# Optimization experiments

Measured on AMD Instinct MI355X. Metric: run time of the kernel, lower is better.

## Reference

```python
import jax, jax.numpy as jnp
import numpy as np
import itertools, math

M_MODES = 10
N_PHOT = 5
IN_MODES = np.array([0, 2, 4, 6, 8])  # input_state = [1,0,1,0,...], 5 photons
INV_SQRT2 = 0.7071067811865476

# Fock output bases (lexicographic ordering)
ROWS_NB = np.array(list(itertools.combinations(range(M_MODES), N_PHOT)), np.int32)          # [252,5] no-bunching
ROWS_B = np.array(list(itertools.combinations_with_replacement(range(M_MODES), N_PHOT)), np.int32)  # [2002,5] bunched

def _norms(rows):
    out = []
    for r in rows:
        c = np.bincount(r, minlength=M_MODES)
        out.append(float(np.prod([math.factorial(int(v)) for v in c])))
    return np.array(out, np.float32)

NORM_NB = _norms(ROWS_NB)  # all ones
NORM_B = _norms(ROWS_B)

# Glynn sign vectors for n=5 permanents (delta_0 fixed to +1): [16,5]
_D = np.array(list(itertools.product([1.0, -1.0], repeat=N_PHOT - 1)), np.float32)
DELTAS = np.concatenate([np.ones((_D.shape[0], 1), np.float32), _D], axis=1)
DSIGNS = np.prod(DELTAS, axis=1)


def _mzi(t1, t2):
    # BS // PS(t1) // BS // PS(t2); BS = (1/sqrt2)[[1,i],[i,1]], PS on first mode of pair
    B = jnp.array([[1.0, 1.0j], [1.0j, 1.0]], dtype=jnp.complex64) * INV_SQRT2
    e1 = jnp.exp(1j * t1)
    e2 = jnp.exp(1j * t2)
    M1 = B * jnp.stack([e1, jnp.ones_like(e1)])[:, None]   # PS(t1) @ BS
    M2 = B @ M1                                            # BS @ ...
    return M2 * jnp.stack([e2, jnp.ones_like(e2)])[:, None]  # PS(t2) @ ...


def interferometer(phases):
    """Rectangular (Clements) mesh on 10 modes with 45 MZIs; phases [45,2] -> U [10,10] complex."""
    Ts = jax.vmap(lambda p: _mzi(p[0], p[1]))(phases)  # [45,2,2]
    U = jnp.eye(M_MODES, dtype=jnp.complex64)
    k = 0
    for layer in range(M_MODES):
        for p in range(layer % 2, M_MODES - 1, 2):
            U = U.at[p:p + 2, :].set(Ts[k] @ U[p:p + 2, :])
            k += 1
    return U


def batched_permanent(Ms):
    """Glynn formula for [...,5,5] complex matrices."""
    D = jnp.asarray(DELTAS, dtype=Ms.dtype)       # [16,5]
    s = jnp.asarray(DSIGNS, dtype=Ms.dtype)       # [16]
    rowsum = jnp.einsum('di,...ij->...dj', D, Ms)  # [...,16,5]
    return jnp.einsum('d,...d->...', s, jnp.prod(rowsum, axis=-1)) / (2 ** (N_PHOT - 1))


def fock_probs(U, rows, norm):
    """U [B,10,10]; rows [K,5] output-mode indices (with repetition for bunching); norm [K]."""
    M = U[:, rows][..., IN_MODES]        # [B,K,5,5]
    perm = batched_permanent(M)          # [B,K]
    return (jnp.abs(perm) ** 2) / jnp.asarray(norm)


def _forward(x, W_down, b_down, phases_l1, phases_r1, phases_lf, phases_rf, W_out, b_out):
    h = (x @ W_down + b_down) / jnp.pi                 # downscale + DivideByPi -> [B,10]
    WL1 = interferometer(phases_l1)
    WR1 = interferometer(phases_r1)
    U1 = jnp.einsum('mk,bk,kn->bmn', WR1, jnp.exp(1j * h), WL1)  # WR @ diag(e^{i phi}) @ WL
    e1 = fock_probs(U1, ROWS_NB, NORM_NB)              # [B,252], no_bunching=True
    # final circuit: 252 px phase shifters round-robin over 10 modes -> phases add per mode
    Bsz = e1.shape[0]
    pad = jnp.pad(e1, ((0, 0), (0, 260 - 252)))
    phi2 = pad.reshape(Bsz, 26, M_MODES).sum(axis=1)   # [B,10]
    WLF = interferometer(phases_lf)
    WRF = interferometer(phases_rf)
    UF = jnp.einsum('mk,bk,kn->bmn', WRF, jnp.exp(1j * phi2), WLF)
    probs = fock_probs(UF, ROWS_B, NORM_B)             # [B,2002], bunched Fock states
    return probs @ W_out + b_out                       # [B,num_classes]


def setup_inputs() -> dict:
    key = jax.random.key(0)
    ks = jax.random.split(key, 9)
    two_pi = 2.0 * np.pi
    return {
        'x': jax.random.normal(ks[0], (128, 784), dtype=jnp.float32),
        'W_down': jax.random.normal(ks[1], (784, 10), dtype=jnp.float32) * 0.05,
        'b_down': jax.random.normal(ks[2], (10,), dtype=jnp.float32) * 0.05,
        'phases_l1': jax.random.uniform(ks[3], (45, 2), dtype=jnp.float32) * two_pi,
        'phases_r1': jax.random.uniform(ks[4], (45, 2), dtype=jnp.float32) * two_pi,
        'phases_lf': jax.random.uniform(ks[5], (45, 2), dtype=jnp.float32) * two_pi,
        'phases_rf': jax.random.uniform(ks[6], (45, 2), dtype=jnp.float32) * two_pi,
        'W_out': jax.random.normal(ks[7], (2002, 10), dtype=jnp.float32) * 0.02,
        'b_out': jax.random.normal(ks[8], (10,), dtype=jnp.float32) * 0.02,
    }


def reference(x, W_down, b_down, phases_l1, phases_r1, phases_lf, phases_rf, W_out, b_out):
    return _forward(x, W_down, b_down, phases_l1, phases_r1, phases_lf, phases_rf, W_out, b_out)
```

## Files before the change

### kernel.cpp

```cpp
#include <hip/hip_runtime.h>
#include <math.h>


#define PI_F 3.14159265358979323846f

__constant__ int BINOM[14][5] = {
  {1, 0, 0, 0, 0},  {1, 1, 0, 0, 0},  {1, 2, 1, 0, 0},   {1, 3, 3, 1, 0},
  {1, 4, 6, 4, 1},  {1, 5,10,10, 5},  {1, 6,15,20,15},   {1, 7,21,35,35},
  {1, 8,28,56,70},  {1, 9,36,84,126}, {1,10,45,120,210}, {1,11,55,165,330},
  {1,12,66,220,495},{1,13,78,286,715}
};
__constant__ float FACTF[6] = {1.f, 1.f, 2.f, 6.f, 24.f, 120.f};

__device__ __forceinline__ float2 cmul(float2 a, float2 b) {
  return make_float2(fmaf(a.x, b.x, -a.y * b.y), fmaf(a.x, b.y, a.y * b.x));
}
__device__ __forceinline__ float2 cadd(float2 a, float2 b) {
  return make_float2(a.x + b.x, a.y + b.y);
}
__device__ __forceinline__ float2 cscale(float2 a, float s) {
  return make_float2(a.x * s, a.y * s);
}
__device__ __forceinline__ float2 imul(float2 a) {
  return make_float2(-a.y, a.x);
}

template <int N>
__device__ __forceinline__ void unrank5(int r, int c[5]) {
  int x = 0;
#pragma unroll
  for (int i = 0; i < 5; i++) {
    for (;;) {
      int cnt = BINOM[N - 1 - x][4 - i];
      if (r < cnt) { c[i] = x; x++; break; }
      r -= cnt; x++;
    }
  }
}

__device__ __forceinline__ float2 perm5(const float2 M[5][5]) {
  float2 rs[5];
#pragma unroll
  for (int j = 0; j < 5; j++) {
    rs[j] = M[0][j];
#pragma unroll
    for (int i = 1; i < 5; i++) rs[j] = cadd(rs[j], M[i][j]);
  }
  float2 acc = cmul(cmul(cmul(cmul(rs[0], rs[1]), rs[2]), rs[3]), rs[4]);
#pragma unroll
  for (int t = 1; t < 16; t++) {
    const int g = t ^ (t >> 1);
    const int bit = (t & 1) ? 0 : ((t & 2) ? 1 : ((t & 4) ? 2 : 3));
    const int i = bit + 1;
    const float step = ((g >> bit) & 1) ? -2.0f : 2.0f;
#pragma unroll
    for (int j = 0; j < 5; j++) {
      rs[j].x = fmaf(step, M[i][j].x, rs[j].x);
      rs[j].y = fmaf(step, M[i][j].y, rs[j].y);
    }
    float2 p = cmul(cmul(cmul(cmul(rs[0], rs[1]), rs[2]), rs[3]), rs[4]);
    const float s = (__popc(g) & 1) ? -1.0f : 1.0f;
    acc.x = fmaf(s, p.x, acc.x);
    acc.y = fmaf(s, p.y, acc.y);
  }
  return make_float2(acc.x * (1.0f / 16.0f), acc.y * (1.0f / 16.0f));
}

__global__ __launch_bounds__(256) void k_head(
    const float* __restrict__ x, const float* __restrict__ Wd,
    const float* __restrict__ bd, const float* __restrict__ ph_l1,
    const float* __restrict__ ph_r1, const float* __restrict__ ph_lf,
    const float* __restrict__ ph_rf, float* __restrict__ h,
    float2* __restrict__ Umats) {
  const int tid = threadIdx.x;
  __shared__ float red[4][10];
  __shared__ float2 T[45][4];
  __shared__ float2 U[100];

  if (blockIdx.x < 128) {
    const int b = blockIdx.x;
    float acc[10];
#pragma unroll
    for (int c = 0; c < 10; c++) acc[c] = 0.f;
    for (int i = tid; i < 784; i += 256) {
      float xv = x[b * 784 + i];
      const float* w = Wd + i * 10;
#pragma unroll
      for (int c = 0; c < 10; c++) acc[c] = fmaf(xv, w[c], acc[c]);
    }
    const int lane = tid & 63, wave = tid >> 6;
#pragma unroll
    for (int c = 0; c < 10; c++) {
      float r = acc[c];
#pragma unroll
      for (int d = 32; d > 0; d >>= 1) r += __shfl_down(r, d);
      if (lane == 0) red[wave][c] = r;
    }
    __syncthreads();
    if (tid < 10) {
      float s = red[0][tid] + red[1][tid] + red[2][tid] + red[3][tid] + bd[tid];
      h[b * 10 + tid] = s * (1.0f / PI_F);
    }
  } else {
    const int which = blockIdx.x - 128;
    const float* ph = (which == 0) ? ph_l1
                    : (which == 1) ? ph_r1
                    : (which == 2) ? ph_lf : ph_rf;
    if (tid < 45) {
      float t1 = ph[tid * 2 + 0], t2 = ph[tid * 2 + 1];
      float s1, c1, s2, c2;
      sincosf(t1, &s1, &c1);
      sincosf(t2, &s2, &c2);
      float2 e2 = make_float2(c2, s2);
      float2 e1m = make_float2(c1 - 1.f, s1);
      float2 e1p = make_float2(c1 + 1.f, s1);
      T[tid][0] = cscale(cmul(e2, e1m), 0.5f);
      T[tid][1] = cscale(cmul(e2, imul(e1p)), 0.5f);
      T[tid][2] = cscale(imul(e1p), 0.5f);
      T[tid][3] = make_float2(0.5f * (1.f - c1), -0.5f * s1);
    }
    if (tid < 100) U[tid] = make_float2((tid % 11 == 0) ? 1.f : 0.f, 0.f);
    __syncthreads();
    int kb = 0;
    for (int layer = 0; layer < 10; layer++) {
      const int start = layer & 1;
      const int npairs = 5 - start;
      if (tid < npairs * 10) {
        const int pi = tid / 10, n = tid % 10;
        const int p = start + 2 * pi;
        const int k = kb + pi;
        float2 u0 = U[p * 10 + n], u1 = U[(p + 1) * 10 + n];
        float2 n0 = cadd(cmul(T[k][0], u0), cmul(T[k][1], u1));
        float2 n1 = cadd(cmul(T[k][2], u0), cmul(T[k][3], u1));
        U[p * 10 + n] = n0;
        U[(p + 1) * 10 + n] = n1;
      }
      kb += npairs;
      __syncthreads();
    }
    if (tid < 100) Umats[which * 100 + tid] = U[tid];
  }
}

__device__ __forceinline__ void buildU(const float2* __restrict__ WRg,
                                       const float2* __restrict__ WLg,
                                       const float2* v, float2* __restrict__ outU,
                                       int tid, float2* A, float2* WLs) {
  if (tid < 100) {
    A[tid] = cmul(WRg[tid], v[tid % 10]);
    WLs[tid] = WLg[tid];
  }
  __syncthreads();
  if (tid < 100) {
    const int m = tid / 10, n = tid % 10;
    float2 acc = make_float2(0.f, 0.f);
#pragma unroll
    for (int k = 0; k < 10; k++)
      acc = cadd(acc, cmul(A[m * 10 + k], WLs[k * 10 + n]));
    outU[tid] = acc;
  }
}

__global__ __launch_bounds__(128) void k_u1(const float* __restrict__ h,
                                            const float2* __restrict__ Umats,
                                            float2* __restrict__ U1) {
  const int b = blockIdx.x, tid = threadIdx.x;
  __shared__ float2 v[10];
  __shared__ float2 A[100];
  __shared__ float2 WLs[100];
  if (tid < 10) {
    float s, c;
    sincosf(h[b * 10 + tid], &s, &c);
    v[tid] = make_float2(c, s);
  }
  __syncthreads();
  buildU(Umats + 100 , Umats + 0 , v, U1 + b * 100, tid, A, WLs);
}

__global__ __launch_bounds__(256) void k_e1(const float2* __restrict__ U1,
                                            float* __restrict__ e1) {
  const int b = blockIdx.x, tid = threadIdx.x;
  __shared__ float2 U[100];
  if (tid < 100) U[tid] = U1[b * 100 + tid];
  __syncthreads();
  if (tid < 252) {
    int c[5];
    unrank5<10>(tid, c);
    float2 M[5][5];
#pragma unroll
    for (int i = 0; i < 5; i++)
#pragma unroll
      for (int j = 0; j < 5; j++) M[i][j] = U[c[i] * 10 + 2 * j];
    float2 p = perm5(M);
    e1[b * 252 + tid] = p.x * p.x + p.y * p.y;
  }
}

__global__ __launch_bounds__(128) void k_uf(const float* __restrict__ e1,
                                            const float2* __restrict__ Umats,
                                            float2* __restrict__ UF) {
  const int b = blockIdx.x, tid = threadIdx.x;
  __shared__ float2 v[10];
  __shared__ float2 A[100];
  __shared__ float2 WLs[100];
  if (tid < 10) {
    float s = 0.f;
    for (int idx = tid; idx < 252; idx += 10) s += e1[b * 252 + idx];
    float sn, cs;
    sincosf(s, &sn, &cs);
    v[tid] = make_float2(cs, sn);
  }
  __syncthreads();
  buildU(Umats + 300 , Umats + 200 , v, UF + b * 100, tid, A, WLs);
}

__global__ __launch_bounds__(256) void k_probs(const float2* __restrict__ UF,
                                               float* __restrict__ probs) {
  const int b = blockIdx.y, tid = threadIdx.x;
  const int k = blockIdx.x * 256 + tid;
  __shared__ float2 U[100];
  if (tid < 100) U[tid] = UF[b * 100 + tid];
  __syncthreads();
  if (k < 2002) {
    int c[5];
    unrank5<14>(k, c);
    int modes[5];
#pragma unroll
    for (int i = 0; i < 5; i++) modes[i] = c[i] - i;
    float2 M[5][5];
#pragma unroll
    for (int i = 0; i < 5; i++)
#pragma unroll
      for (int j = 0; j < 5; j++) M[i][j] = U[modes[i] * 10 + 2 * j];
    float2 p = perm5(M);
    float norm = 1.f;
    int run = 1;
#pragma unroll
    for (int i = 1; i < 5; i++) {
      if (modes[i] == modes[i - 1]) run++;
      else { norm *= FACTF[run]; run = 1; }
    }
    norm *= FACTF[run];
    probs[b * 2002 + k] = (p.x * p.x + p.y * p.y) / norm;
  }
}

__global__ __launch_bounds__(256) void k_out(const float* __restrict__ probs,
                                             const float* __restrict__ Wout,
                                             const float* __restrict__ bout,
                                             float* __restrict__ out) {
  const int b = blockIdx.x, tid = threadIdx.x;
  __shared__ float red[4][10];
  float acc[10];
#pragma unroll
  for (int c = 0; c < 10; c++) acc[c] = 0.f;
  for (int k = tid; k < 2002; k += 256) {
    float p = probs[b * 2002 + k];
    const float* w = Wout + k * 10;
#pragma unroll
    for (int c = 0; c < 10; c++) acc[c] = fmaf(p, w[c], acc[c]);
  }
  const int lane = tid & 63, wave = tid >> 6;
#pragma unroll
  for (int c = 0; c < 10; c++) {
    float r = acc[c];
#pragma unroll
    for (int d = 32; d > 0; d >>= 1) r += __shfl_down(r, d);
    if (lane == 0) red[wave][c] = r;
  }
  __syncthreads();
  if (tid < 10) {
    float s = red[0][tid] + red[1][tid] + red[2][tid] + red[3][tid];
    out[b * 10 + tid] = s + bout[tid];
  }
}

extern "C" void kernel_launch(void* const* d_in, const int* in_sizes, int n_in,
                              void* d_out, int out_size, void* d_ws,
                              size_t ws_size, hipStream_t stream) {
  const float* x    = (const float*)d_in[0];
  const float* Wd   = (const float*)d_in[1];
  const float* bd   = (const float*)d_in[2];
  const float* pl1  = (const float*)d_in[3];
  const float* pr1  = (const float*)d_in[4];
  const float* plf  = (const float*)d_in[5];
  const float* prf  = (const float*)d_in[6];
  const float* Wout = (const float*)d_in[7];
  const float* bout = (const float*)d_in[8];
  float* out = (float*)d_out;

  float* ws = (float*)d_ws;
  float*  h     = ws;
  float2* Umats = (float2*)(ws + 1280);
  float2* U1    = (float2*)(ws + 2080);
  float*  e1    = ws + 27680;
  float2* UF    = (float2*)(ws + 59936);
  float*  probs = ws + 85536;

  k_head <<<132, 256, 0, stream>>>(x, Wd, bd, pl1, pr1, plf, prf, h, Umats);
  k_u1   <<<128, 128, 0, stream>>>(h, Umats, U1);
  k_e1   <<<128, 256, 0, stream>>>(U1, e1);
  k_uf   <<<128, 128, 0, stream>>>(e1, Umats, UF);
  k_probs<<<dim3(8, 128), 256, 0, stream>>>(UF, probs);
  k_out  <<<128, 256, 0, stream>>>(probs, Wout, bout, out);
}
```

Measured before the change: 102.1 us.

## Fuse six-kernel pipeline into a single per-sample kernel

All six stages (downprojection, interferometer construction, U1 build, no-bunching permanents, UF build, bunched permanents plus output matvec) now run in one kernel with one block per batch sample, keeping intermediates in shared memory. Each block redundantly recomputes the four interferometer matrices, and the bunched-probability stage loops over 8 chunks per thread instead of using 8 blocks per sample. This removes five kernel launches and the global round trips for the intermediates. In exchange, the probs stage now runs on only 128 blocks, which reduces parallelism for the heaviest stage.

```diff
diff --git a/kernel.cpp b/kernel.cpp
--- a/kernel.cpp
+++ b/kernel.cpp
@@ -66,123 +66,106 @@
   return make_float2(acc.x * (1.0f / 16.0f), acc.y * (1.0f / 16.0f));
 }
 
-__global__ __launch_bounds__(256) void k_head(
+__global__ __launch_bounds__(256) void k_fused(
     const float* __restrict__ x, const float* __restrict__ Wd,
     const float* __restrict__ bd, const float* __restrict__ ph_l1,
     const float* __restrict__ ph_r1, const float* __restrict__ ph_lf,
-    const float* __restrict__ ph_rf, float* __restrict__ h,
-    float2* __restrict__ Umats) {
-  const int tid = threadIdx.x;
-  __shared__ float red[4][10];
-  __shared__ float2 T[45][4];
-  __shared__ float2 U[100];
-
-  if (blockIdx.x < 128) {
-    const int b = blockIdx.x;
-    float acc[10];
-#pragma unroll
-    for (int c = 0; c < 10; c++) acc[c] = 0.f;
-    for (int i = tid; i < 784; i += 256) {
-      float xv = x[b * 784 + i];
-      const float* w = Wd + i * 10;
-#pragma unroll
-      for (int c = 0; c < 10; c++) acc[c] = fmaf(xv, w[c], acc[c]);
-    }
-    const int lane = tid & 63, wave = tid >> 6;
-#pragma unroll
-    for (int c = 0; c < 10; c++) {
-      float r = acc[c];
-#pragma unroll
-      for (int d = 32; d > 0; d >>= 1) r += __shfl_down(r, d);
-      if (lane == 0) red[wave][c] = r;
-    }
-    __syncthreads();
-    if (tid < 10) {
-      float s = red[0][tid] + red[1][tid] + red[2][tid] + red[3][tid] + bd[tid];
-      h[b * 10 + tid] = s * (1.0f / PI_F);
-    }
-  } else {
-    const int which = blockIdx.x - 128;
+    const float* __restrict__ ph_rf, const float* __restrict__ Wout,
+    const float* __restrict__ bout, float* __restrict__ out) {
+  const int b = blockIdx.x, tid = threadIdx.x;
+
+  __shared__ float2 T[4][45][4];
+  __shared__ float2 Ui[4][100];
+  __shared__ float2 A[100];
+  __shared__ float2 Ub[100];
+  __shared__ float  e1s[252];
+  __shared__ float  red[4][10];
+  __shared__ float2 v[10];
+
+  float hacc[10];
+#pragma unroll
+  for (int c = 0; c < 10; c++) hacc[c] = 0.f;
+  for (int i = tid; i < 784; i += 256) {
+    float xv = x[b * 784 + i];
+    const float* w = Wd + i * 10;
+#pragma unroll
+    for (int c = 0; c < 10; c++) hacc[c] = fmaf(xv, w[c], hacc[c]);
+  }
+
+  if (tid < 180) {
+    const int which = tid / 45, m = tid % 45;
     const float* ph = (which == 0) ? ph_l1
                     : (which == 1) ? ph_r1
                     : (which == 2) ? ph_lf : ph_rf;
-    if (tid < 45) {
-      float t1 = ph[tid * 2 + 0], t2 = ph[tid * 2 + 1];
-      float s1, c1, s2, c2;
-      sincosf(t1, &s1, &c1);
-      sincosf(t2, &s2, &c2);
-      float2 e2 = make_float2(c2, s2);
-      float2 e1m = make_float2(c1 - 1.f, s1);
-      float2 e1p = make_float2(c1 + 1.f, s1);
-      T[tid][0] = cscale(cmul(e2, e1m), 0.5f);
-      T[tid][1] = cscale(cmul(e2, imul(e1p)), 0.5f);
-      T[tid][2] = cscale(imul(e1p), 0.5f);
-      T[tid][3] = make_float2(0.5f * (1.f - c1), -0.5f * s1);
-    }
-    if (tid < 100) U[tid] = make_float2((tid % 11 == 0) ? 1.f : 0.f, 0.f);
+    float t1 = ph[m * 2 + 0], t2 = ph[m * 2 + 1];
+    float s1, c1, s2, c2;
+    sincosf(t1, &s1, &c1);
+    sincosf(t2, &s2, &c2);
+    float2 e2  = make_float2(c2, s2);
+    float2 e1m = make_float2(c1 - 1.f, s1);
+    float2 e1p = make_float2(c1 + 1.f, s1);
+    T[which][m][0] = cscale(cmul(e2, e1m), 0.5f);
+    T[which][m][1] = cscale(cmul(e2, imul(e1p)), 0.5f);
+    T[which][m][2] = cscale(imul(e1p), 0.5f);
+    T[which][m][3] = make_float2(0.5f * (1.f - c1), -0.5f * s1);
+  }
+  for (int idx = tid; idx < 400; idx += 256)
+    Ui[idx / 100][idx % 100] = make_float2((idx % 100) % 11 == 0 ? 1.f : 0.f, 0.f);
+
+  {
+    const int lane = tid & 63, wave = tid >> 6;
+#pragma unroll
+    for (int c = 0; c < 10; c++) {
+      float r = hacc[c];
+#pragma unroll
+      for (int d = 32; d > 0; d >>= 1) r += __shfl_down(r, d);
+      if (lane == 0) red[wave][c] = r;
+    }
+  }
+
+  int kb = 0;
+  for (int layer = 0; layer < 10; layer++) {
     __syncthreads();
-    int kb = 0;
-    for (int layer = 0; layer < 10; layer++) {
-      const int start = layer & 1;
-      const int npairs = 5 - start;
-      if (tid < npairs * 10) {
-        const int pi = tid / 10, n = tid % 10;
+    const int start = layer & 1;
+    const int npairs = 5 - start;
+    if (tid < 200) {
+      const int which = tid / 50, tl = tid % 50;
+      if (tl < npairs * 10) {
+        const int pi = tl / 10, n = tl % 10;
         const int p = start + 2 * pi;
         const int k = kb + pi;
-        float2 u0 = U[p * 10 + n], u1 = U[(p + 1) * 10 + n];
-        float2 n0 = cadd(cmul(T[k][0], u0), cmul(T[k][1], u1));
-        float2 n1 = cadd(cmul(T[k][2], u0), cmul(T[k][3], u1));
-        U[p * 10 + n] = n0;
-        U[(p + 1) * 10 + n] = n1;
+        float2 u0 = Ui[which][p * 10 + n], u1 = Ui[which][(p + 1) * 10 + n];
+        float2 n0 = cadd(cmul(T[which][k][0], u0), cmul(T[which][k][1], u1));
+        float2 n1 = cadd(cmul(T[which][k][2], u0), cmul(T[which][k][3], u1));
+        Ui[which][p * 10 + n] = n0;
+        Ui[which][(p + 1) * 10 + n] = n1;
       }
-      kb += npairs;
-      __syncthreads();
-    }
-    if (tid < 100) Umats[which * 100 + tid] = U[tid];
-  }
-}
-
-__device__ __forceinline__ void buildU(const float2* __restrict__ WRg,
-                                       const float2* __restrict__ WLg,
-                                       const float2* v, float2* __restrict__ outU,
-                                       int tid, float2* A, float2* WLs) {
-  if (tid < 100) {
-    A[tid] = cmul(WRg[tid], v[tid % 10]);
-    WLs[tid] = WLg[tid];
-  }
+    }
+    kb += npairs;
+  }
+  __syncthreads();
+
+  if (tid < 10) {
+    float s = red[0][tid] + red[1][tid] + red[2][tid] + red[3][tid] + bd[tid];
+    s *= (1.0f / PI_F);
+    float sn, cs;
+    sincosf(s, &sn, &cs);
+    v[tid] = make_float2(cs, sn);
+  }
+  __syncthreads();
+
+  if (tid < 100) A[tid] = cmul(Ui[1][tid], v[tid % 10]);
   __syncthreads();
   if (tid < 100) {
     const int m = tid / 10, n = tid % 10;
     float2 acc = make_float2(0.f, 0.f);
 #pragma unroll
     for (int k = 0; k < 10; k++)
-      acc = cadd(acc, cmul(A[m * 10 + k], WLs[k * 10 + n]));
-    outU[tid] = acc;
-  }
-}
-
-__global__ __launch_bounds__(128) void k_u1(const float* __restrict__ h,
-                                            const float2* __restrict__ Umats,
-                                            float2* __restrict__ U1) {
-  const int b = blockIdx.x, tid = threadIdx.x;
-  __shared__ float2 v[10];
-  __shared__ float2 A[100];
-  __shared__ float2 WLs[100];
-  if (tid < 10) {
-    float s, c;
-    sincosf(h[b * 10 + tid], &s, &c);
-    v[tid] = make_float2(c, s);
-  }
-  __syncthreads();
-  buildU(Umats + 100 , Umats + 0 , v, U1 + b * 100, tid, A, WLs);
-}
-
-__global__ __launch_bounds__(256) void k_e1(const float2* __restrict__ U1,
-                                            float* __restrict__ e1) {
-  const int b = blockIdx.x, tid = threadIdx.x;
-  __shared__ float2 U[100];
-  if (tid < 100) U[tid] = U1[b * 100 + tid];
-  __syncthreads();
+      acc = cadd(acc, cmul(A[m * 10 + k], Ui[0][k * 10 + n]));
+    Ub[tid] = acc;
+  }
+  __syncthreads();
+
   if (tid < 252) {
     int c[5];
     unrank5<10>(tid, c);
@@ -190,83 +173,75 @@
 #pragma unroll
     for (int i = 0; i < 5; i++)
 #pragma unroll
-      for (int j = 0; j < 5; j++) M[i][j] = U[c[i] * 10 + 2 * j];
+      for (int j = 0; j < 5; j++) M[i][j] = Ub[c[i] * 10 + 2 * j];
     float2 p = perm5(M);
-    e1[b * 252 + tid] = p.x * p.x + p.y * p.y;
-  }
-}
-
-__global__ __launch_bounds__(128) void k_uf(const float* __restrict__ e1,
-                                            const float2* __restrict__ Umats,
-                                            float2* __restrict__ UF) {
-  const int b = blockIdx.x, tid = threadIdx.x;
-  __shared__ float2 v[10];
-  __shared__ float2 A[100];
-  __shared__ float2 WLs[100];
+    e1s[tid] = p.x * p.x + p.y * p.y;
+  }
+  __syncthreads();
+
   if (tid < 10) {
     float s = 0.f;
-    for (int idx = tid; idx < 252; idx += 10) s += e1[b * 252 + idx];
+    for (int idx = tid; idx < 252; idx += 10) s += e1s[idx];
     float sn, cs;
     sincosf(s, &sn, &cs);
     v[tid] = make_float2(cs, sn);
   }
   __syncthreads();
-  buildU(Umats + 300 , Umats + 200 , v, UF + b * 100, tid, A, WLs);
-}
-
-__global__ __launch_bounds__(256) void k_probs(const float2* __restrict__ UF,
-                                               float* __restrict__ probs) {
-  const int b = blockIdx.y, tid = threadIdx.x;
-  const int k = blockIdx.x * 256 + tid;
-  __shared__ float2 U[100];
-  if (tid < 100) U[tid] = UF[b * 100 + tid];
-  __syncthreads();
-  if (k < 2002) {
-    int c[5];
-    unrank5<14>(k, c);
-    int modes[5];
-#pragma unroll
-    for (int i = 0; i < 5; i++) modes[i] = c[i] - i;
-    float2 M[5][5];
-#pragma unroll
-    for (int i = 0; i < 5; i++)
-#pragma unroll
-      for (int j = 0; j < 5; j++) M[i][j] = U[modes[i] * 10 + 2 * j];
-    float2 p = perm5(M);
-    float norm = 1.f;
-    int run = 1;
-#pragma unroll
-    for (int i = 1; i < 5; i++) {
-      if (modes[i] == modes[i - 1]) run++;
-      else { norm *= FACTF[run]; run = 1; }
-    }
-    norm *= FACTF[run];
-    probs[b * 2002 + k] = (p.x * p.x + p.y * p.y) / norm;
-  }
-}
-
-__global__ __launch_bounds__(256) void k_out(const float* __restrict__ probs,
-                                             const float* __restrict__ Wout,
-                                             const float* __restrict__ bout,
-                                             float* __restrict__ out) {
-  const int b = blockIdx.x, tid = threadIdx.x;
-  __shared__ float red[4][10];
+
+  if (tid < 100) A[tid] = cmul(Ui[3][tid], v[tid % 10]);
+  __syncthreads();
+  if (tid < 100) {
+    const int m = tid / 10, n = tid % 10;
+    float2 acc = make_float2(0.f, 0.f);
+#pragma unroll
+    for (int k = 0; k < 10; k++)
+      acc = cadd(acc, cmul(A[m * 10 + k], Ui[2][k * 10 + n]));
+    Ub[tid] = acc;
+  }
+  __syncthreads();
+
   float acc[10];
 #pragma unroll
   for (int c = 0; c < 10; c++) acc[c] = 0.f;
-  for (int k = tid; k < 2002; k += 256) {
-    float p = probs[b * 2002 + k];
-    const float* w = Wout + k * 10;
-#pragma unroll
-    for (int c = 0; c < 10; c++) acc[c] = fmaf(p, w[c], acc[c]);
-  }
-  const int lane = tid & 63, wave = tid >> 6;
-#pragma unroll
-  for (int c = 0; c < 10; c++) {
-    float r = acc[c];
-#pragma unroll
-    for (int d = 32; d > 0; d >>= 1) r += __shfl_down(r, d);
-    if (lane == 0) red[wave][c] = r;
+#pragma unroll
+  for (int it = 0; it < 8; it++) {
+    const int k = tid + it * 256;
+    if (k < 2002) {
+      int c5[5];
+      unrank5<14>(k, c5);
+      int modes[5];
+#pragma unroll
+      for (int i = 0; i < 5; i++) modes[i] = c5[i] - i;
+      float2 M[5][5];
+#pragma unroll
+      for (int i = 0; i < 5; i++)
+#pragma unroll
+        for (int j = 0; j < 5; j++) M[i][j] = Ub[modes[i] * 10 + 2 * j];
+      float2 p = perm5(M);
+      float norm = 1.f;
+      int run = 1;
+#pragma unroll
+      for (int i = 1; i < 5; i++) {
+        if (modes[i] == modes[i - 1]) run++;
+        else { norm *= FACTF[run]; run = 1; }
+      }
+      norm *= FACTF[run];
+      const float pv = (p.x * p.x + p.y * p.y) / norm;
+      const float* w = Wout + k * 10;
+#pragma unroll
+      for (int c = 0; c < 10; c++) acc[c] = fmaf(pv, w[c], acc[c]);
+    }
+  }
+
+  {
+    const int lane = tid & 63, wave = tid >> 6;
+#pragma unroll
+    for (int c = 0; c < 10; c++) {
+      float r = acc[c];
+#pragma unroll
+      for (int d = 32; d > 0; d >>= 1) r += __shfl_down(r, d);
+      if (lane == 0) red[wave][c] = r;
+    }
   }
   __syncthreads();
   if (tid < 10) {
@@ -289,18 +264,6 @@
   const float* bout = (const float*)d_in[8];
   float* out = (float*)d_out;
 
-  float* ws = (float*)d_ws;
-  float*  h     = ws;
-  float2* Umats = (float2*)(ws + 1280);
-  float2* U1    = (float2*)(ws + 2080);
-  float*  e1    = ws + 27680;
-  float2* UF    = (float2*)(ws + 59936);
-  float*  probs = ws + 85536;
-
-  k_head <<<132, 256, 0, stream>>>(x, Wd, bd, pl1, pr1, plf, prf, h, Umats);
-  k_u1   <<<128, 128, 0, stream>>>(h, Umats, U1);
-  k_e1   <<<128, 256, 0, stream>>>(U1, e1);
-  k_uf   <<<128, 128, 0, stream>>>(e1, Umats, UF);
-  k_probs<<<dim3(8, 128), 256, 0, stream>>>(UF, probs);
-  k_out  <<<128, 256, 0, stream>>>(probs, Wout, bout, out);
-}
+  k_fused<<<128, 256, 0, stream>>>(x, Wd, bd, pl1, pr1, plf, prf, Wout, bout,
+                                   out);
+}
```

Result: slower. 110.6 us (+8.3%).
